# Kernel tuning notes

Measured on AMD Instinct MI355X. Metric: run time of the kernel, lower is better.

The kernel has to match this reference:

```python
import jax, jax.numpy as jnp
import numpy as np

N, E, G = 65536, 524288, 1024
ND, ED, HID, H, C = 21, 12, 128, 4, 32
L = 8  # num_blocks * 2 conv layers
EPS = 1e-5


def _gatv2(x, src, dst, ea, Wl, Wr, We, att, bias):
    # PyG GATv2Conv: xl=lin_l(x) (source), xr=lin_r(x) (target)
    n = x.shape[0]
    xl = jnp.einsum('nd,dhc->nhc', x, Wl)   # [N,H,C]
    xr = jnp.einsum('nd,dhc->nhc', x, Wr)
    el = jnp.einsum('ed,dhc->ehc', ea, We)  # [E,H,C]
    m = xl[src] + xr[dst] + el              # per-edge message pre-activation
    e = jnp.einsum('ehc,hc->eh', jax.nn.leaky_relu(m, 0.2), att)  # [E,H]
    # scatter softmax over incoming edges of each dst node
    emax = jax.ops.segment_max(e, dst, num_segments=n)
    emax = jnp.where(jnp.isfinite(emax), emax, 0.0)
    p = jnp.exp(e - emax[dst])
    denom = jax.ops.segment_sum(p, dst, num_segments=n)
    alpha = p / jnp.clip(denom, 1e-16)[dst]
    out = jax.ops.segment_sum(alpha[..., None] * xl[src], dst, num_segments=n)
    return out.reshape(n, H * C) + bias


def _bn(x, scale, bias):
    mu = x.mean(0)
    var = x.var(0)
    return (x - mu) * jax.lax.rsqrt(var + EPS) * scale + bias


def setup_inputs():
    key = jax.random.key(0)
    ks = jax.random.split(key, 16)
    f = lambda k, shp, s=0.05: jax.random.normal(k, shp, jnp.float32) * s
    return dict(
        x=f(ks[0], (N, ND), 1.0),
        edge_attr=f(ks[1], (E, ED), 1.0),
        edge_index=jax.random.randint(ks[2], (2, E), 0, N),
        batch=jnp.sort(jax.random.randint(ks[3], (N,), 0, G)),
        Win=f(ks[4], (ND, HID)), bin_=jnp.zeros(HID),
        Wl=f(ks[5], (L, HID, H, C)), Wr=f(ks[6], (L, HID, H, C)),
        We=f(ks[7], (L, ED, H, C)), att=f(ks[8], (L, H, C)),
        bconv=jnp.zeros((L, HID)),
        bn_scale=jnp.ones((L, HID)), bn_bias=jnp.zeros((L, HID)),
        Wv1=f(ks[9], (HID, 64)), bv1=jnp.zeros(64),
        Wv2=f(ks[10], (64, 3)), bv2=jnp.zeros(3),
        Wp1=f(ks[11], (2 * HID + ED, 64)), bp1=jnp.zeros(64),
        Wp2=f(ks[12], (64, 1)), bp2=jnp.zeros(1),
    )


def reference(x, edge_attr, edge_index, batch, Win, bin_, Wl, Wr, We, att,
              bconv, bn_scale, bn_bias, Wv1, bv1, Wv2, bv2, Wp1, bp1, Wp2, bp2):
    src0, dst0 = edge_index[0], edge_index[1]
    # add_self_loops with fill_value='mean' for edge features
    ones_e = jnp.ones((E,), x.dtype)
    deg = jax.ops.segment_sum(ones_e, dst0, num_segments=N)
    mean_ea = jax.ops.segment_sum(edge_attr, dst0, num_segments=N) / jnp.clip(deg, 1.0)[:, None]
    ar = jnp.arange(N)
    src = jnp.concatenate([src0, ar])
    dst = jnp.concatenate([dst0, ar])
    ea = jnp.concatenate([edge_attr, mean_ea], axis=0)

    h = jax.nn.relu(x @ Win + bin_)
    for b in range(L // 2):
        i, j = 2 * b, 2 * b + 1
        res = h
        h = _gatv2(h, src, dst, ea, Wl[i], Wr[i], We[i], att[i], bconv[i])
        h = jax.nn.relu(_bn(h, bn_scale[i], bn_bias[i]))
        h = _gatv2(h, src, dst, ea, Wl[j], Wr[j], We[j], att[j], bconv[j])
        h = _bn(h, bn_scale[j], bn_bias[j])
        h = jax.nn.relu(h + res)

    counts = jax.ops.segment_sum(jnp.ones((N,), h.dtype), batch, num_segments=G)
    pooled = jax.ops.segment_sum(h, batch, num_segments=G) / jnp.clip(counts, 1.0)[:, None]
    value_logits = jax.nn.relu(pooled @ Wv1 + bv1) @ Wv2 + bv2  # [G,3]

    edge_input = jnp.concatenate([h[src0], h[dst0], edge_attr], axis=1)  # [E, 2*HID+ED]
    policy_logits = (jax.nn.relu(edge_input @ Wp1 + bp1) @ Wp2 + bp2)[:, 0]  # [E]
    return value_logits, policy_logits
```

## Files before the change

### kernel.cpp

```cpp
#include <hip/hip_runtime.h>
#include <hip/hip_fp16.h>

#define NN 65536
#define EE 524288
#define EPX 589824
#define GG 1024
#define NSLOT 32

typedef __attribute__((ext_vector_type(8))) short bf16x8;
typedef __attribute__((ext_vector_type(4))) float f32x4;

#define LOG2E 1.44269504088896f


__device__ __forceinline__ unsigned short f2bf(float x) {
    unsigned int u = __float_as_uint(x);
    u += 0x7FFFu + ((u >> 16) & 1u);
    return (unsigned short)(u >> 16);
}
__device__ __forceinline__ float bflo(unsigned int w) { return __uint_as_float(w << 16); }
__device__ __forceinline__ float bfhi(unsigned int w) { return __uint_as_float(w & 0xFFFF0000u); }
__device__ __forceinline__ float bf2f(unsigned short u) { return __uint_as_float((unsigned int)u << 16); }
__device__ __forceinline__ float lrelu(float x) { return fmaf(0.4f, fabsf(x), 0.6f * x); }
__device__ __forceinline__ unsigned int packh2(float a, float b) {
    __half2 h = __floats2half2_rn(a, b);
    return *reinterpret_cast<unsigned int*>(&h);
}
__device__ __forceinline__ unsigned long long rfl64(unsigned long long v) {
    unsigned int lo = __builtin_amdgcn_readfirstlane((unsigned int)v);
    unsigned int hi = __builtin_amdgcn_readfirstlane((unsigned int)(v >> 32));
    return (((unsigned long long)hi) << 32) | lo;
}

template <int CTRL>
__device__ __forceinline__ float dpp_add(float v) {
    int x = __builtin_amdgcn_update_dpp(0, __float_as_int(v), CTRL, 0xf, 0xf, true);
    return v + __int_as_float(x);
}
__device__ __forceinline__ float head_reduce(float t) {
    t = dpp_add<0xB1>(t);
    t = dpp_add<0x4E>(t);
    t = dpp_add<0x124>(t);
    t = dpp_add<0x128>(t);
    return t;
}


__launch_bounds__(256)
__global__ void k_deg(const int* __restrict__ dst0, int* __restrict__ deg)
{
    int e = blockIdx.x * 256 + threadIdx.x;
    if (e >= EE) return;
    atomicAdd(&deg[dst0[e]], 1);
}

__launch_bounds__(1024)
__global__ void k_scan(const int* __restrict__ deg, int* __restrict__ rowptr)
{
    __shared__ int sums[1024];
    int t = threadIdx.x;
    int base = t * 64;
    int s = 0;
    for (int i = 0; i < 64; i++) s += deg[base + i] + 1;
    sums[t] = s;
    __syncthreads();
    for (int off = 1; off < 1024; off <<= 1) {
        int v = (t >= off) ? sums[t - off] : 0;
        __syncthreads();
        sums[t] += v;
        __syncthreads();
    }
    int off = sums[t] - s;
    for (int i = 0; i < 64; i++) { rowptr[base + i] = off; off += deg[base + i] + 1; }
    if (t == 1023) rowptr[NN] = off;
}

__launch_bounds__(256)
__global__ void k_scatter(const int* __restrict__ src0, const int* __restrict__ dst0,
                          const float* __restrict__ eattr,
                          const int* __restrict__ rowptr, const int* __restrict__ deg,
                          int* __restrict__ fill, int* __restrict__ csr_src,
                          unsigned short* __restrict__ eaCSR,
                          unsigned short* __restrict__ eaOrd)
{
    int e = blockIdx.x * 256 + threadIdx.x;
    if (e >= EPX) return;
    if (e < EE) {
        int d = dst0[e];
        int pos = rowptr[d] + atomicAdd(&fill[d], 1);
        csr_src[pos] = src0[e] << 8;
        const float* ep = eattr + (size_t)e * 12;
        float4 a = *reinterpret_cast<const float4*>(ep);
        float4 b = *reinterpret_cast<const float4*>(ep + 4);
        float4 c = *reinterpret_cast<const float4*>(ep + 8);
        uint4 w; w.x = packh2(a.x, a.y); w.y = packh2(a.z, a.w);
        w.z = packh2(b.x, b.y); w.w = packh2(b.z, b.w);
        uint2 w2 = make_uint2(packh2(c.x, c.y), packh2(c.z, c.w));
        unsigned short* o = eaCSR + (size_t)pos * 16;
        *reinterpret_cast<uint4*>(o) = w;
        *reinterpret_cast<uint2*>(o + 8) = w2;
        unsigned short* o2 = eaOrd + (size_t)e * 16;
        *reinterpret_cast<uint4*>(o2) = w;
        *reinterpret_cast<uint2*>(o2 + 8) = w2;
    } else {
        int n = e - EE;
        csr_src[rowptr[n] + deg[n]] = n << 8;
    }
}

__launch_bounds__(256)
__global__ void k_selfattr(const int* __restrict__ rowptr, unsigned short* __restrict__ eaCSR)
{
    int tid = blockIdx.x * 256 + threadIdx.x;
    int n = tid >> 4;
    int lk = tid & 15;
    if (lk >= 12) return;
    int beg = rowptr[n], endm1 = rowptr[n + 1] - 1;
    float s = 0.f;
    for (int p = beg; p < endm1; ++p) {
        __half h = *reinterpret_cast<const __half*>(&eaCSR[(size_t)p * 16 + lk]);
        s += __half2float(h);
    }
    float dv = fmaxf((float)(endm1 - beg), 1.0f);
    __half ho = __float2half(s / dv);
    eaCSR[(size_t)endm1 * 16 + lk] = *reinterpret_cast<unsigned short*>(&ho);
}


__launch_bounds__(256)
__global__ void k_wprep(const float* __restrict__ Wl, const float* __restrict__ Wr,
                        const float* __restrict__ Wp1,
                        unsigned short* __restrict__ wg, unsigned short* __restrict__ wp)
{
    int tid = blockIdx.x * 256 + threadIdx.x;
    if (tid < 32768) {
        int l = tid >> 12;
        int r = tid & 4095;
        int kt = r >> 10, ct = (r >> 6) & 15, lane = r & 63;
        int kb = kt * 32 + (lane >> 4) * 8;
        int col = ct * 16 + (lane & 15);
        const float* W = (col < 128) ? (Wl + (size_t)l * 16384 + col)
                                     : (Wr + (size_t)l * 16384 + (col - 128));
        unsigned short* o = wg + (size_t)tid * 8;
#pragma unroll
        for (int j = 0; j < 8; j++) o[j] = f2bf(W[(size_t)(kb + j) * 128]);
    } else if (tid < 34816) {
        int r = tid - 32768;
        int kt = r >> 9, ct = (r >> 6) & 7, lane = r & 63;
        int kb = kt * 32 + (lane >> 4) * 8;
        int col = ct * 16 + (lane & 15);
        const float* W = (col < 64) ? (Wp1 + col) : (Wp1 + 128 * 64 + (col - 64));
        unsigned short* o = wp + (size_t)r * 8;
#pragma unroll
        for (int j = 0; j < 8; j++) o[j] = f2bf(W[(size_t)(kb + j) * 64]);
    }
}


__launch_bounds__(256)
__global__ void k_input(const float* __restrict__ x, const float* __restrict__ Win,
                        const float* __restrict__ bin, float* __restrict__ h)
{
    __shared__ float W[21 * 128];
    int t = threadIdx.x;
    for (int i = t; i < 21 * 128; i += 256) W[i] = Win[i];
    __syncthreads();
    int c = t & 127, sub = t >> 7;
    int n0 = blockIdx.x * 16;
    float bc = bin[c];
    for (int i = 0; i < 8; i++) {
        int n = n0 + sub + i * 2;
        const float* xp = x + (size_t)n * 21;
        float acc = bc;
#pragma unroll
        for (int k = 0; k < 21; k++) acc = fmaf(xp[k], W[k * 128 + c], acc);
        h[(size_t)n * 128 + c] = fmaxf(acc, 0.f);
    }
}


__device__ __forceinline__ void load_afrag(const float* __restrict__ A, int arow, int kb,
                                           bf16x8 af[4])
{
#pragma unroll
    for (int kt = 0; kt < 4; kt++) {
        const float* ap = A + (size_t)arow * 128 + kt * 32 + kb;
        float4 lo = *reinterpret_cast<const float4*>(ap);
        float4 hi = *reinterpret_cast<const float4*>(ap + 4);
        bf16x8 v;
        v[0] = (short)f2bf(lo.x); v[1] = (short)f2bf(lo.y);
        v[2] = (short)f2bf(lo.z); v[3] = (short)f2bf(lo.w);
        v[4] = (short)f2bf(hi.x); v[5] = (short)f2bf(hi.y);
        v[6] = (short)f2bf(hi.z); v[7] = (short)f2bf(hi.w);
        af[kt] = v;
    }
}

__device__ __forceinline__ void gemm_gat_core(const bf16x8 af[4], const unsigned short* __restrict__ Bf,
                                              int row0, unsigned short* __restrict__ Cl,
                                              unsigned short* __restrict__ Cr, int lane)
{
    int crow = row0 + (lane >> 4) * 4;
    int c0 = lane & 15;
#pragma unroll
    for (int ct = 0; ct < 16; ct++) {
        f32x4 acc = {0.f, 0.f, 0.f, 0.f};
#pragma unroll
        for (int kt = 0; kt < 4; kt++) {
            bf16x8 bf = *reinterpret_cast<const bf16x8*>(Bf + ((size_t)(kt * 16 + ct) * 64 + lane) * 8);
            acc = __builtin_amdgcn_mfma_f32_16x16x32_bf16(af[kt], bf, acc, 0, 0, 0);
        }
        int col = ct * 16 + c0;
        unsigned short* C = (col < 128) ? Cl : Cr;
        int cc = col & 127;
#pragma unroll
        for (int r = 0; r < 4; r++)
            C[(size_t)(crow + r) * 128 + cc] = f2bf(acc[r]);
    }
}

__launch_bounds__(256)
__global__ void k_gemm_gat(const float* __restrict__ A, const unsigned short* __restrict__ Bf,
                           unsigned short* __restrict__ Cl, unsigned short* __restrict__ Cr)
{
    int wave = threadIdx.x >> 6, lane = threadIdx.x & 63;
    int row0 = blockIdx.x * 64 + wave * 16;
    bf16x8 af[4];
    load_afrag(A, row0 + (lane & 15), (lane >> 4) * 8, af);
    gemm_gat_core(af, Bf, row0, Cl, Cr, lane);
}

__launch_bounds__(256)
__global__ void k_gemm_gat_bn(const float* __restrict__ G, const float* __restrict__ bnstat,
                              const float* __restrict__ scale, const float* __restrict__ bias,
                              const unsigned short* __restrict__ Bf,
                              unsigned short* __restrict__ Cl, unsigned short* __restrict__ Cr)
{
    __shared__ float sA[128], bA[128];
    int t = threadIdx.x;
    if (t < 128) {
        float sum = 0.f, sq = 0.f;
#pragma unroll
        for (int sl = 0; sl < NSLOT; sl++) {
            sum += bnstat[sl * 256 + t];
            sq  += bnstat[sl * 256 + 128 + t];
        }
        const float invN = 1.0f / (float)NN;
        float mean = sum * invN;
        float var  = sq * invN - mean * mean;
        float sc   = scale[t] * rsqrtf(var + 1e-5f);
        sA[t] = sc;
        bA[t] = bias[t] - mean * sc;
    }
    __syncthreads();
    int wave = t >> 6, lane = t & 63;
    int row0 = blockIdx.x * 64 + wave * 16;
    int arow = row0 + (lane & 15);
    int kb = (lane >> 4) * 8;
    bf16x8 af[4];
#pragma unroll
    for (int kt = 0; kt < 4; kt++) {
        int cb = kt * 32 + kb;
        const float* gp = G + (size_t)arow * 128 + cb;
        float4 lo = *reinterpret_cast<const float4*>(gp);
        float4 hi = *reinterpret_cast<const float4*>(gp + 4);
        bf16x8 v;
        v[0] = (short)f2bf(fmaxf(fmaf(lo.x, sA[cb + 0], bA[cb + 0]), 0.f));
        v[1] = (short)f2bf(fmaxf(fmaf(lo.y, sA[cb + 1], bA[cb + 1]), 0.f));
        v[2] = (short)f2bf(fmaxf(fmaf(lo.z, sA[cb + 2], bA[cb + 2]), 0.f));
        v[3] = (short)f2bf(fmaxf(fmaf(lo.w, sA[cb + 3], bA[cb + 3]), 0.f));
        v[4] = (short)f2bf(fmaxf(fmaf(hi.x, sA[cb + 4], bA[cb + 4]), 0.f));
        v[5] = (short)f2bf(fmaxf(fmaf(hi.y, sA[cb + 5], bA[cb + 5]), 0.f));
        v[6] = (short)f2bf(fmaxf(fmaf(hi.z, sA[cb + 6], bA[cb + 6]), 0.f));
        v[7] = (short)f2bf(fmaxf(fmaf(hi.w, sA[cb + 7], bA[cb + 7]), 0.f));
        af[kt] = v;
    }
    gemm_gat_core(af, Bf, row0, Cl, Cr, lane);
}

__launch_bounds__(256)
__global__ void k_gemm_pol(const float* __restrict__ A, const unsigned short* __restrict__ Bf,
                           unsigned short* __restrict__ P)
{
    int wave = threadIdx.x >> 6, lane = threadIdx.x & 63;
    int row0 = blockIdx.x * 64 + wave * 16;
    bf16x8 af[4];
    load_afrag(A, row0 + (lane & 15), (lane >> 4) * 8, af);
    int crow = row0 + (lane >> 4) * 4;
    int c0 = lane & 15;
#pragma unroll
    for (int ct = 0; ct < 8; ct++) {
        f32x4 acc = {0.f, 0.f, 0.f, 0.f};
#pragma unroll
        for (int kt = 0; kt < 4; kt++) {
            bf16x8 bf = *reinterpret_cast<const bf16x8*>(Bf + ((size_t)(kt * 8 + ct) * 64 + lane) * 8);
            acc = __builtin_amdgcn_mfma_f32_16x16x32_bf16(af[kt], bf, acc, 0, 0, 0);
        }
        int col = ct * 16 + c0;
#pragma unroll
        for (int r = 0; r < 4; r++)
            P[(size_t)(crow + r) * 128 + col] = f2bf(acc[r]);
    }
}


__device__ __forceinline__ float2 edge_el(uint4 A, uint2 C,
                                          const __half2 wx[6], const __half2 wy[6])
{
    __half2 e0 = *reinterpret_cast<const __half2*>(&A.x);
    __half2 e1 = *reinterpret_cast<const __half2*>(&A.y);
    __half2 e2 = *reinterpret_cast<const __half2*>(&A.z);
    __half2 e3 = *reinterpret_cast<const __half2*>(&A.w);
    __half2 e4 = *reinterpret_cast<const __half2*>(&C.x);
    __half2 e5 = *reinterpret_cast<const __half2*>(&C.y);
    __half2 ax = __hmul2(e0, wx[0]);
    ax = __hfma2(e1, wx[1], ax); ax = __hfma2(e2, wx[2], ax);
    ax = __hfma2(e3, wx[3], ax); ax = __hfma2(e4, wx[4], ax);
    ax = __hfma2(e5, wx[5], ax);
    __half2 ay = __hmul2(e0, wy[0]);
    ay = __hfma2(e1, wy[1], ay); ay = __hfma2(e2, wy[2], ay);
    ay = __hfma2(e3, wy[3], ay); ay = __hfma2(e4, wy[4], ay);
    ay = __hfma2(e5, wy[5], ay);
    float2 r;
    r.x = __half2float(__hadd(__low2half(ax), __high2half(ax)));
    r.y = __half2float(__hadd(__low2half(ay), __high2half(ay)));
    return r;
}

__launch_bounds__(256)
__global__ void k_gat(const unsigned short* __restrict__ xlb, const unsigned short* __restrict__ xrb,
                      const unsigned short* __restrict__ eaCSR,
                      const int* __restrict__ rowptr, const int* __restrict__ csr_src,
                      const float* __restrict__ We, const float* __restrict__ att,
                      const float* __restrict__ bconv, float* __restrict__ g,
                      float* __restrict__ bnstat)
{
    int wid = blockIdx.x * 4 + (threadIdx.x >> 6);
    int lane = threadIdx.x & 63;
    int f0 = lane * 2;

    const int* cs_s = (const int*)rfl64((unsigned long long)csr_src);
    const unsigned short* ea_s = (const unsigned short*)rfl64((unsigned long long)eaCSR);

    __half2 wx[6], wy[6];
#pragma unroll
    for (int j = 0; j < 6; j++) {
        float2 w0 = *reinterpret_cast<const float2*>(We + (2 * j) * 128 + f0);
        float2 w1 = *reinterpret_cast<const float2*>(We + (2 * j + 1) * 128 + f0);
        wx[j] = __floats2half2_rn(w0.x, w1.x);
        wy[j] = __floats2half2_rn(w0.y, w1.y);
    }
    float2 av = *reinterpret_cast<const float2*>(att + f0);
    av.x *= LOG2E; av.y *= LOG2E;
    float2 bc = *reinterpret_cast<const float2*>(bconv + f0);
    const char* xl_lane = reinterpret_cast<const char*>(xlb) + (lane << 2);

    float bs0 = 0.f, bs1 = 0.f, bq0 = 0.f, bq1 = 0.f;

    for (int n = wid * 4; n < wid * 4 + 4; ++n) {
        unsigned int xrw = *reinterpret_cast<const unsigned int*>(xrb + (size_t)n * 128 + f0);
        float xr0 = bflo(xrw), xr1 = bfhi(xrw);

        float sA_ = 0.f, a0A = 0.f, a1A = 0.f;
        float sB_ = 0.f, a0B = 0.f, a1B = 0.f;
        int beg = rowptr[n], end = rowptr[n + 1];
        int idx = beg;
        for (; idx + 4 <= end; idx += 4) {
            int off0 = cs_s[idx],     off1 = cs_s[idx + 1];
            int off2 = cs_s[idx + 2], off3 = cs_s[idx + 3];
            const unsigned short* ep = ea_s + (size_t)idx * 16;
            uint4 qA = *reinterpret_cast<const uint4*>(ep);
            uint2 qC = *reinterpret_cast<const uint2*>(ep + 8);
            uint4 rA = *reinterpret_cast<const uint4*>(ep + 16);
            uint2 rC = *reinterpret_cast<const uint2*>(ep + 24);
            uint4 sAq = *reinterpret_cast<const uint4*>(ep + 32);
            uint2 sC = *reinterpret_cast<const uint2*>(ep + 40);
            uint4 tA = *reinterpret_cast<const uint4*>(ep + 48);
            uint2 tC = *reinterpret_cast<const uint2*>(ep + 56);
            unsigned int xw0 = *reinterpret_cast<const unsigned int*>(xl_lane + off0);
            unsigned int xw1 = *reinterpret_cast<const unsigned int*>(xl_lane + off1);
            unsigned int xw2 = *reinterpret_cast<const unsigned int*>(xl_lane + off2);
            unsigned int xw3 = *reinterpret_cast<const unsigned int*>(xl_lane + off3);

            float2 el0 = edge_el(qA, qC, wx, wy);
            float2 el1 = edge_el(rA, rC, wx, wy);
            float2 el2 = edge_el(sAq, sC, wx, wy);
            float2 el3 = edge_el(tA, tC, wx, wy);

            float xa0 = bflo(xw0), xa1 = bfhi(xw0);
            float xb0 = bflo(xw1), xb1 = bfhi(xw1);
            float xc0 = bflo(xw2), xc1 = bfhi(xw2);
            float xd0 = bflo(xw3), xd1 = bfhi(xw3);

            float t0 = lrelu(xa0 + xr0 + el0.x) * av.x + lrelu(xa1 + xr1 + el0.y) * av.y;
            float t1 = lrelu(xb0 + xr0 + el1.x) * av.x + lrelu(xb1 + xr1 + el1.y) * av.y;
            float t2 = lrelu(xc0 + xr0 + el2.x) * av.x + lrelu(xc1 + xr1 + el2.y) * av.y;
            float t3 = lrelu(xd0 + xr0 + el3.x) * av.x + lrelu(xd1 + xr1 + el3.y) * av.y;
            t0 = head_reduce(t0); t1 = head_reduce(t1);
            t2 = head_reduce(t2); t3 = head_reduce(t3);

            float w0 = exp2f(t0);
            float w1 = exp2f(t1);
            float w2 = exp2f(t2);
            float w3 = exp2f(t3);
            sA_ += w0 + w1;
            sB_ += w2 + w3;
            a0A = fmaf(w0, xa0, fmaf(w1, xb0, a0A));
            a1A = fmaf(w0, xa1, fmaf(w1, xb1, a1A));
            a0B = fmaf(w2, xc0, fmaf(w3, xd0, a0B));
            a1B = fmaf(w2, xc1, fmaf(w3, xd1, a1B));
        }
        for (; idx < end; ++idx) {
            int off0 = cs_s[idx];
            const unsigned short* ep = ea_s + (size_t)idx * 16;
            uint4 qA = *reinterpret_cast<const uint4*>(ep);
            uint2 qC = *reinterpret_cast<const uint2*>(ep + 8);
            unsigned int xw0 = *reinterpret_cast<const unsigned int*>(xl_lane + off0);
            float2 el0 = edge_el(qA, qC, wx, wy);
            float xa0 = bflo(xw0), xa1 = bfhi(xw0);
            float tt = lrelu(xa0 + xr0 + el0.x) * av.x + lrelu(xa1 + xr1 + el0.y) * av.y;
            tt = head_reduce(tt);
            float w = exp2f(tt);
            sA_ += w;
            a0A = fmaf(w, xa0, a0A);
            a1A = fmaf(w, xa1, a1A);
        }
        float s  = sA_ + sB_;
        float a0 = a0A + a0B;
        float a1 = a1A + a1B;
        float inv = 1.f / s;
        float r0 = fmaf(a0, inv, bc.x);
        float r1 = fmaf(a1, inv, bc.y);
        *reinterpret_cast<float2*>(g + (size_t)n * 128 + f0) = make_float2(r0, r1);
        bs0 += r0; bs1 += r1;
        bq0 = fmaf(r0, r0, bq0); bq1 = fmaf(r1, r1, bq1);
    }

    __shared__ float red[256 * 4];
    int t = threadIdx.x;
    red[t * 4 + 0] = bs0; red[t * 4 + 1] = bs1;
    red[t * 4 + 2] = bq0; red[t * 4 + 3] = bq1;
    __syncthreads();
    if (t < 64) {
        float v0 = red[t * 4 + 0] + red[(t + 64) * 4 + 0] + red[(t + 128) * 4 + 0] + red[(t + 192) * 4 + 0];
        float v1 = red[t * 4 + 1] + red[(t + 64) * 4 + 1] + red[(t + 128) * 4 + 1] + red[(t + 192) * 4 + 1];
        float q0 = red[t * 4 + 2] + red[(t + 64) * 4 + 2] + red[(t + 128) * 4 + 2] + red[(t + 192) * 4 + 2];
        float q1 = red[t * 4 + 3] + red[(t + 64) * 4 + 3] + red[(t + 128) * 4 + 3] + red[(t + 192) * 4 + 3];
        float* slot = bnstat + (size_t)(blockIdx.x & (NSLOT - 1)) * 256;
        atomicAdd(&slot[2 * t + 0], v0);
        atomicAdd(&slot[2 * t + 1], v1);
        atomicAdd(&slot[128 + 2 * t + 0], q0);
        atomicAdd(&slot[128 + 2 * t + 1], q1);
    }
}


__launch_bounds__(256)
__global__ void k_bnapply_res_relu(const float4* __restrict__ gin,
                                   const float* __restrict__ bnstat,
                                   const float* __restrict__ scale, const float* __restrict__ bias,
                                   float4* __restrict__ hbuf)
{
    __shared__ float sA[128], bA[128];
    int t = threadIdx.x;
    if (t < 128) {
        float sum = 0.f, sq = 0.f;
#pragma unroll
        for (int sl = 0; sl < NSLOT; sl++) {
            sum += bnstat[sl * 256 + t];
            sq  += bnstat[sl * 256 + 128 + t];
        }
        const float invN = 1.0f / (float)NN;
        float mean = sum * invN;
        float var  = sq * invN - mean * mean;
        float sc   = scale[t] * rsqrtf(var + 1e-5f);
        sA[t] = sc;
        bA[t] = bias[t] - mean * sc;
    }
    __syncthreads();
    int idx = blockIdx.x * 256 + t;
    int c4 = (idx & 31) * 4;
    float4 v = gin[idx];
    float4 hv = hbuf[idx];
    float4 r;
    r.x = fmaxf(fmaf(v.x, sA[c4 + 0], bA[c4 + 0]) + hv.x, 0.f);
    r.y = fmaxf(fmaf(v.y, sA[c4 + 1], bA[c4 + 1]) + hv.y, 0.f);
    r.z = fmaxf(fmaf(v.z, sA[c4 + 2], bA[c4 + 2]) + hv.z, 0.f);
    r.w = fmaxf(fmaf(v.w, sA[c4 + 3], bA[c4 + 3]) + hv.w, 0.f);
    hbuf[idx] = r;
}


__launch_bounds__(128)
__global__ void k_pool(const float* __restrict__ h, const int* __restrict__ batch,
                       float* __restrict__ pooled, float* __restrict__ cnt)
{
    int c = threadIdx.x;
    int r0 = blockIdx.x * 128;
    int cur = batch[r0];
    float acc = 0.f;
    float run = 0.f;
    for (int i = 0; i < 128; ++i) {
        int r = r0 + i;
        int b = batch[r];
        if (b != cur) {
            atomicAdd(&pooled[(size_t)cur * 128 + c], acc);
            if (c == 0) atomicAdd(&cnt[cur], run);
            acc = 0.f; run = 0.f; cur = b;
        }
        acc += h[(size_t)r * 128 + c];
        run += 1.f;
    }
    atomicAdd(&pooled[(size_t)cur * 128 + c], acc);
    if (c == 0) atomicAdd(&cnt[cur], run);
}

__launch_bounds__(64)
__global__ void k_value(const float* __restrict__ pooled, const float* __restrict__ cnt,
                        const float* __restrict__ Wv1, const float* __restrict__ bv1,
                        const float* __restrict__ Wv2, const float* __restrict__ bv2,
                        float* __restrict__ out)
{
    int gi = blockIdx.x;
    int l = threadIdx.x;
    float inv = 1.f / fmaxf(cnt[gi], 1.f);
    const float* pr = pooled + (size_t)gi * 128;
    float z = bv1[l];
    for (int k = 0; k < 128; k++) z = fmaf(pr[k] * inv, Wv1[k * 64 + l], z);
    z = fmaxf(z, 0.f);
#pragma unroll
    for (int j = 0; j < 3; j++) {
        float p = z * Wv2[l * 3 + j];
        p += __shfl_xor(p, 32); p += __shfl_xor(p, 16); p += __shfl_xor(p, 8);
        p += __shfl_xor(p, 4);  p += __shfl_xor(p, 2);  p += __shfl_xor(p, 1);
        if (l == 0) out[gi * 3 + j] = p + bv2[j];
    }
}


__device__ __forceinline__ void dec12(uint4 A, uint2 C, float* o)
{
    __half2 h;
    h = *reinterpret_cast<__half2*>(&A.x); o[0] = __low2float(h); o[1]  = __high2float(h);
    h = *reinterpret_cast<__half2*>(&A.y); o[2] = __low2float(h); o[3]  = __high2float(h);
    h = *reinterpret_cast<__half2*>(&A.z); o[4] = __low2float(h); o[5]  = __high2float(h);
    h = *reinterpret_cast<__half2*>(&A.w); o[6] = __low2float(h); o[7]  = __high2float(h);
    h = *reinterpret_cast<__half2*>(&C.x); o[8] = __low2float(h); o[9]  = __high2float(h);
    h = *reinterpret_cast<__half2*>(&C.y); o[10] = __low2float(h); o[11] = __high2float(h);
}

__launch_bounds__(256)
__global__ void k_policy(const unsigned short* __restrict__ P,
                         const unsigned short* __restrict__ eaOrd,
                         const int* __restrict__ src0, const int* __restrict__ dst0,
                         const float* __restrict__ Wp1c, const float* __restrict__ bp1,
                         const float* __restrict__ Wp2, const float* __restrict__ bp2,
                         float* __restrict__ out)
{
    int wave = (blockIdx.x * 256 + threadIdx.x) >> 6;
    int lane = threadIdx.x & 63;
    const unsigned short* ea_s = (const unsigned short*)rfl64((unsigned long long)eaOrd);
    const int* s_s = (const int*)rfl64((unsigned long long)src0);
    const int* d_s = (const int*)rfl64((unsigned long long)dst0);
    float w1c[12];
#pragma unroll
    for (int k = 0; k < 12; k++) w1c[k] = Wp1c[k * 64 + lane];
    float wp2 = Wp2[lane];
    float bb = bp1[lane];
    float b2 = bp2[0];
    for (int i = 0; i < 8; i += 2) {
        int e0i = wave * 8 + i;
        int e1i = e0i + 1;
        int sI0 = s_s[e0i], dI0 = d_s[e0i];
        int sI1 = s_s[e1i], dI1 = d_s[e1i];
        const unsigned short* ep = ea_s + (size_t)e0i * 16;
        uint4 A0 = *reinterpret_cast<const uint4*>(ep);
        uint2 C0 = *reinterpret_cast<const uint2*>(ep + 8);
        uint4 A1 = *reinterpret_cast<const uint4*>(ep + 16);
        uint2 C1 = *reinterpret_cast<const uint2*>(ep + 24);
        unsigned short ps0 = P[(size_t)sI0 * 128 + lane];
        unsigned short pd0 = P[(size_t)dI0 * 128 + 64 + lane];
        unsigned short ps1 = P[(size_t)sI1 * 128 + lane];
        unsigned short pd1 = P[(size_t)dI1 * 128 + 64 + lane];

        float ea0[12], ea1[12];
        dec12(A0, C0, ea0);
        dec12(A1, C1, ea1);

        float z0 = bf2f(ps0) + bf2f(pd0) + bb;
        float z1 = bf2f(ps1) + bf2f(pd1) + bb;
#pragma unroll
        for (int k = 0; k < 12; k++) {
            z0 = fmaf(ea0[k], w1c[k], z0);
            z1 = fmaf(ea1[k], w1c[k], z1);
        }
        float p0 = fmaxf(z0, 0.f) * wp2;
        float p1 = fmaxf(z1, 0.f) * wp2;
        p0 = head_reduce(p0);
        p1 = head_reduce(p1);
        p0 += __shfl_xor(p0, 16); p1 += __shfl_xor(p1, 16);
        p0 += __shfl_xor(p0, 32); p1 += __shfl_xor(p1, 32);
        if (lane == 0) {
            out[3072 + e0i] = p0 + b2;
            out[3072 + e1i] = p1 + b2;
        }
    }
}


extern "C" void kernel_launch(void* const* d_in, const int* in_sizes, int n_in,
                              void* d_out, int out_size, void* d_ws, size_t ws_size,
                              hipStream_t stream)
{
    const float* x     = (const float*)d_in[0];
    const float* eattr = (const float*)d_in[1];
    const int*   eidx  = (const int*)d_in[2];
    const int*   batch = (const int*)d_in[3];
    const float* Win   = (const float*)d_in[4];
    const float* bin   = (const float*)d_in[5];
    const float* Wl    = (const float*)d_in[6];
    const float* Wr    = (const float*)d_in[7];
    const float* We    = (const float*)d_in[8];
    const float* att   = (const float*)d_in[9];
    const float* bconv = (const float*)d_in[10];
    const float* bnsc  = (const float*)d_in[11];
    const float* bnbi  = (const float*)d_in[12];
    const float* Wv1   = (const float*)d_in[13];
    const float* bv1   = (const float*)d_in[14];
    const float* Wv2   = (const float*)d_in[15];
    const float* bv2   = (const float*)d_in[16];
    const float* Wp1   = (const float*)d_in[17];
    const float* bp1   = (const float*)d_in[18];
    const float* Wp2   = (const float*)d_in[19];
    const float* bp2   = (const float*)d_in[20];
    float* out = (float*)d_out;

    const int* src0 = eidx;
    const int* dst0 = eidx + EE;

    const size_t NH = (size_t)NN * 128;
    float* ws = (float*)d_ws;
    float* h  = ws;
    float* g  = h + NH;
    unsigned short* xlb = (unsigned short*)(g + NH);
    unsigned short* xrb = xlb + NH;
    unsigned short* eaCSR = xrb + NH;
    unsigned short* eaOrd = eaCSR + (size_t)EPX * 16;
    int* rowptr = (int*)(eaOrd + (size_t)EE * 16);
    int* csr_src = rowptr + (NN + 1);
    int* deg  = csr_src + EPX;
    int* fill = deg + NN;
    float* bnstat = (float*)(fill + NN);
    float* pooled = bnstat + 8 * NSLOT * 256;
    float* cnt    = pooled + (size_t)GG * 128;
    size_t zero_elems = (size_t)NN + NN + 8 * NSLOT * 256 + (size_t)GG * 128 + GG;
    unsigned short* wg = (unsigned short*)(cnt + GG);
    unsigned short* wp = wg + 8 * 32768;

    hipMemsetAsync(deg, 0, zero_elems * sizeof(float), stream);

    k_deg<<<EE / 256, 256, 0, stream>>>(dst0, deg);
    k_scan<<<1, 1024, 0, stream>>>(deg, rowptr);
    k_scatter<<<EPX / 256, 256, 0, stream>>>(src0, dst0, eattr, rowptr, deg, fill,
                                             csr_src, eaCSR, eaOrd);
    k_selfattr<<<(NN * 16) / 256, 256, 0, stream>>>(rowptr, eaCSR);
    k_wprep<<<136, 256, 0, stream>>>(Wl, Wr, Wp1, wg, wp);

    k_input<<<NN / 16, 256, 0, stream>>>(x, Win, bin, h);

    for (int l = 0; l < 8; l++) {
        float* bs = bnstat + (size_t)l * NSLOT * 256;
        if (l % 2 == 0) {
            k_gemm_gat<<<NN / 64, 256, 0, stream>>>(h, wg + (size_t)l * 32768, xlb, xrb);
        } else {
            float* bsp = bnstat + (size_t)(l - 1) * NSLOT * 256;
            k_gemm_gat_bn<<<NN / 64, 256, 0, stream>>>(g, bsp,
                                                       bnsc + (size_t)(l - 1) * 128,
                                                       bnbi + (size_t)(l - 1) * 128,
                                                       wg + (size_t)l * 32768, xlb, xrb);
        }
        k_gat<<<NN / 16, 256, 0, stream>>>(xlb, xrb, eaCSR, rowptr, csr_src,
                                           We + (size_t)l * 1536, att + (size_t)l * 128,
                                           bconv + (size_t)l * 128, g, bs);
        if (l % 2 == 1) {
            k_bnapply_res_relu<<<(NN * 128 / 4) / 256, 256, 0, stream>>>(
                (const float4*)g, bs, bnsc + (size_t)l * 128, bnbi + (size_t)l * 128,
                (float4*)h);
        }
    }

    k_pool<<<NN / 128, 128, 0, stream>>>(h, batch, pooled, cnt);
    k_value<<<GG, 64, 0, stream>>>(pooled, cnt, Wv1, bv1, Wv2, bv2, out);

    unsigned short* P = xlb;
    k_gemm_pol<<<NN / 64, 256, 0, stream>>>(h, wp, P);
    k_policy<<<NN / 4, 256, 0, stream>>>(P, eaOrd, src0, dst0,
                                         Wp1 + 256 * 64, bp1, Wp2, bp2, out);
}
```

Baseline: 1.082 ms.

## Fuse BN-residual-ReLU into next GEMM and use fdot2 for edge features

```diff
diff --git a/kernel.cpp b/kernel.cpp
--- a/kernel.cpp
+++ b/kernel.cpp
@@ -9,8 +9,13 @@
 
 typedef __attribute__((ext_vector_type(8))) short bf16x8;
 typedef __attribute__((ext_vector_type(4))) float f32x4;
+typedef _Float16 f16x2 __attribute__((ext_vector_type(2)));
 
 #define LOG2E 1.44269504088896f
+
+#if __has_builtin(__builtin_amdgcn_fdot2)
+#define HAVE_FDOT2 1
+#endif
 
 
 __device__ __forceinline__ unsigned short f2bf(float x) {
@@ -25,6 +30,17 @@
 __device__ __forceinline__ unsigned int packh2(float a, float b) {
     __half2 h = __floats2half2_rn(a, b);
     return *reinterpret_cast<unsigned int*>(&h);
+}
+__device__ __forceinline__ f16x2 as_f16x2(unsigned int u) {
+    union { unsigned int u; f16x2 h; } c; c.u = u; return c.h;
+}
+__device__ __forceinline__ float fdot2p(unsigned int e, f16x2 w, float acc) {
+#ifdef HAVE_FDOT2
+    return __builtin_amdgcn_fdot2(as_f16x2(e), w, acc, false);
+#else
+    __half2 h = *reinterpret_cast<__half2*>(&e);
+    return acc + __low2float(h) * (float)w[0] + __high2float(h) * (float)w[1];
+#endif
 }
 __device__ __forceinline__ unsigned long long rfl64(unsigned long long v) {
     unsigned int lo = __builtin_amdgcn_readfirstlane((unsigned int)v);
@@ -230,13 +246,11 @@
     gemm_gat_core(af, Bf, row0, Cl, Cr, lane);
 }
 
-__launch_bounds__(256)
-__global__ void k_gemm_gat_bn(const float* __restrict__ G, const float* __restrict__ bnstat,
-                              const float* __restrict__ scale, const float* __restrict__ bias,
-                              const unsigned short* __restrict__ Bf,
-                              unsigned short* __restrict__ Cl, unsigned short* __restrict__ Cr)
-{
-    __shared__ float sA[128], bA[128];
+__device__ __forceinline__ void bn_coeff_lds(const float* __restrict__ bnstat,
+                                             const float* __restrict__ scale,
+                                             const float* __restrict__ bias,
+                                             float* sA, float* bA)
+{
     int t = threadIdx.x;
     if (t < 128) {
         float sum = 0.f, sq = 0.f;
@@ -253,6 +267,17 @@
         bA[t] = bias[t] - mean * sc;
     }
     __syncthreads();
+}
+
+__launch_bounds__(256)
+__global__ void k_gemm_gat_bn(const float* __restrict__ G, const float* __restrict__ bnstat,
+                              const float* __restrict__ scale, const float* __restrict__ bias,
+                              const unsigned short* __restrict__ Bf,
+                              unsigned short* __restrict__ Cl, unsigned short* __restrict__ Cr)
+{
+    __shared__ float sA[128], bA[128];
+    bn_coeff_lds(bnstat, scale, bias, sA, bA);
+    int t = threadIdx.x;
     int wave = t >> 6, lane = t & 63;
     int row0 = blockIdx.x * 64 + wave * 16;
     int arow = row0 + (lane & 15);
@@ -279,6 +304,50 @@
 }
 
 __launch_bounds__(256)
+__global__ void k_gemm_gat_bnres(const float* __restrict__ G, const float* __restrict__ bnstat,
+                                 const float* __restrict__ scale, const float* __restrict__ bias,
+                                 float* __restrict__ H, const unsigned short* __restrict__ Bf,
+                                 unsigned short* __restrict__ Cl, unsigned short* __restrict__ Cr)
+{
+    __shared__ float sA[128], bA[128];
+    bn_coeff_lds(bnstat, scale, bias, sA, bA);
+    int t = threadIdx.x;
+    int wave = t >> 6, lane = t & 63;
+    int row0 = blockIdx.x * 64 + wave * 16;
+    int arow = row0 + (lane & 15);
+    int kb = (lane >> 4) * 8;
+    bf16x8 af[4];
+#pragma unroll
+    for (int kt = 0; kt < 4; kt++) {
+        int cb = kt * 32 + kb;
+        const float* gp = G + (size_t)arow * 128 + cb;
+        float* hp = H + (size_t)arow * 128 + cb;
+        float4 glo = *reinterpret_cast<const float4*>(gp);
+        float4 ghi = *reinterpret_cast<const float4*>(gp + 4);
+        float4 hlo = *reinterpret_cast<const float4*>(hp);
+        float4 hhi = *reinterpret_cast<const float4*>(hp + 4);
+        float4 nlo, nhi;
+        nlo.x = fmaxf(fmaf(glo.x, sA[cb + 0], bA[cb + 0]) + hlo.x, 0.f);
+        nlo.y = fmaxf(fmaf(glo.y, sA[cb + 1], bA[cb + 1]) + hlo.y, 0.f);
+        nlo.z = fmaxf(fmaf(glo.z, sA[cb + 2], bA[cb + 2]) + hlo.z, 0.f);
+        nlo.w = fmaxf(fmaf(glo.w, sA[cb + 3], bA[cb + 3]) + hlo.w, 0.f);
+        nhi.x = fmaxf(fmaf(ghi.x, sA[cb + 4], bA[cb + 4]) + hhi.x, 0.f);
+        nhi.y = fmaxf(fmaf(ghi.y, sA[cb + 5], bA[cb + 5]) + hhi.y, 0.f);
+        nhi.z = fmaxf(fmaf(ghi.z, sA[cb + 6], bA[cb + 6]) + hhi.z, 0.f);
+        nhi.w = fmaxf(fmaf(ghi.w, sA[cb + 7], bA[cb + 7]) + hhi.w, 0.f);
+        *reinterpret_cast<float4*>(hp) = nlo;
+        *reinterpret_cast<float4*>(hp + 4) = nhi;
+        bf16x8 v;
+        v[0] = (short)f2bf(nlo.x); v[1] = (short)f2bf(nlo.y);
+        v[2] = (short)f2bf(nlo.z); v[3] = (short)f2bf(nlo.w);
+        v[4] = (short)f2bf(nhi.x); v[5] = (short)f2bf(nhi.y);
+        v[6] = (short)f2bf(nhi.z); v[7] = (short)f2bf(nhi.w);
+        af[kt] = v;
+    }
+    gemm_gat_core(af, Bf, row0, Cl, Cr, lane);
+}
+
+__launch_bounds__(256)
 __global__ void k_gemm_pol(const float* __restrict__ A, const unsigned short* __restrict__ Bf,
                            unsigned short* __restrict__ P)
 {
@@ -305,25 +374,21 @@
 
 
 __device__ __forceinline__ float2 edge_el(uint4 A, uint2 C,
-                                          const __half2 wx[6], const __half2 wy[6])
-{
-    __half2 e0 = *reinterpret_cast<const __half2*>(&A.x);
-    __half2 e1 = *reinterpret_cast<const __half2*>(&A.y);
-    __half2 e2 = *reinterpret_cast<const __half2*>(&A.z);
-    __half2 e3 = *reinterpret_cast<const __half2*>(&A.w);
-    __half2 e4 = *reinterpret_cast<const __half2*>(&C.x);
-    __half2 e5 = *reinterpret_cast<const __half2*>(&C.y);
-    __half2 ax = __hmul2(e0, wx[0]);
-    ax = __hfma2(e1, wx[1], ax); ax = __hfma2(e2, wx[2], ax);
-    ax = __hfma2(e3, wx[3], ax); ax = __hfma2(e4, wx[4], ax);
-    ax = __hfma2(e5, wx[5], ax);
-    __half2 ay = __hmul2(e0, wy[0]);
-    ay = __hfma2(e1, wy[1], ay); ay = __hfma2(e2, wy[2], ay);
-    ay = __hfma2(e3, wy[3], ay); ay = __hfma2(e4, wy[4], ay);
-    ay = __hfma2(e5, wy[5], ay);
-    float2 r;
-    r.x = __half2float(__hadd(__low2half(ax), __high2half(ax)));
-    r.y = __half2float(__hadd(__low2half(ay), __high2half(ay)));
+                                          const f16x2 wx[6], const f16x2 wy[6])
+{
+    float ex = fdot2p(A.x, wx[0], 0.f);
+    ex = fdot2p(A.y, wx[1], ex);
+    ex = fdot2p(A.z, wx[2], ex);
+    ex = fdot2p(A.w, wx[3], ex);
+    ex = fdot2p(C.x, wx[4], ex);
+    ex = fdot2p(C.y, wx[5], ex);
+    float ey = fdot2p(A.x, wy[0], 0.f);
+    ey = fdot2p(A.y, wy[1], ey);
+    ey = fdot2p(A.z, wy[2], ey);
+    ey = fdot2p(A.w, wy[3], ey);
+    ey = fdot2p(C.x, wy[4], ey);
+    ey = fdot2p(C.y, wy[5], ey);
+    float2 r; r.x = ex; r.y = ey;
     return r;
 }
 
@@ -342,13 +407,13 @@
     const int* cs_s = (const int*)rfl64((unsigned long long)csr_src);
     const unsigned short* ea_s = (const unsigned short*)rfl64((unsigned long long)eaCSR);
 
-    __half2 wx[6], wy[6];
+    f16x2 wx[6], wy[6];
 #pragma unroll
     for (int j = 0; j < 6; j++) {
         float2 w0 = *reinterpret_cast<const float2*>(We + (2 * j) * 128 + f0);
         float2 w1 = *reinterpret_cast<const float2*>(We + (2 * j + 1) * 128 + f0);
-        wx[j] = __floats2half2_rn(w0.x, w1.x);
-        wy[j] = __floats2half2_rn(w0.y, w1.y);
+        wx[j] = (f16x2){(_Float16)w0.x, (_Float16)w1.x};
+        wy[j] = (f16x2){(_Float16)w0.y, (_Float16)w1.y};
     }
     float2 av = *reinterpret_cast<const float2*>(att + f0);
     av.x *= LOG2E; av.y *= LOG2E;
@@ -462,22 +527,8 @@
                                    float4* __restrict__ hbuf)
 {
     __shared__ float sA[128], bA[128];
+    bn_coeff_lds(bnstat, scale, bias, sA, bA);
     int t = threadIdx.x;
-    if (t < 128) {
-        float sum = 0.f, sq = 0.f;
-#pragma unroll
-        for (int sl = 0; sl < NSLOT; sl++) {
-            sum += bnstat[sl * 256 + t];
-            sq  += bnstat[sl * 256 + 128 + t];
-        }
-        const float invN = 1.0f / (float)NN;
-        float mean = sum * invN;
-        float var  = sq * invN - mean * mean;
-        float sc   = scale[t] * rsqrtf(var + 1e-5f);
-        sA[t] = sc;
-        bA[t] = bias[t] - mean * sc;
-    }
-    __syncthreads();
     int idx = blockIdx.x * 256 + t;
     int c4 = (idx & 31) * 4;
     float4 v = gin[idx];
@@ -538,17 +589,6 @@
 }
 
 
-__device__ __forceinline__ void dec12(uint4 A, uint2 C, float* o)
-{
-    __half2 h;
-    h = *reinterpret_cast<__half2*>(&A.x); o[0] = __low2float(h); o[1]  = __high2float(h);
-    h = *reinterpret_cast<__half2*>(&A.y); o[2] = __low2float(h); o[3]  = __high2float(h);
-    h = *reinterpret_cast<__half2*>(&A.z); o[4] = __low2float(h); o[5]  = __high2float(h);
-    h = *reinterpret_cast<__half2*>(&A.w); o[6] = __low2float(h); o[7]  = __high2float(h);
-    h = *reinterpret_cast<__half2*>(&C.x); o[8] = __low2float(h); o[9]  = __high2float(h);
-    h = *reinterpret_cast<__half2*>(&C.y); o[10] = __low2float(h); o[11] = __high2float(h);
-}
-
 __launch_bounds__(256)
 __global__ void k_policy(const unsigned short* __restrict__ P,
                          const unsigned short* __restrict__ eaOrd,
@@ -562,9 +602,10 @@
     const unsigned short* ea_s = (const unsigned short*)rfl64((unsigned long long)eaOrd);
     const int* s_s = (const int*)rfl64((unsigned long long)src0);
     const int* d_s = (const int*)rfl64((unsigned long long)dst0);
-    float w1c[12];
-#pragma unroll
-    for (int k = 0; k < 12; k++) w1c[k] = Wp1c[k * 64 + lane];
+    f16x2 w1h[6];
+#pragma unroll
+    for (int j = 0; j < 6; j++)
+        w1h[j] = (f16x2){(_Float16)Wp1c[(2 * j) * 64 + lane], (_Float16)Wp1c[(2 * j + 1) * 64 + lane]};
     float wp2 = Wp2[lane];
     float bb = bp1[lane];
     float b2 = bp2[0];
@@ -583,17 +624,15 @@
         unsigned short ps1 = P[(size_t)sI1 * 128 + lane];
         unsigned short pd1 = P[(size_t)dI1 * 128 + 64 + lane];
 
-        float ea0[12], ea1[12];
-        dec12(A0, C0, ea0);
-        dec12(A1, C1, ea1);
-
         float z0 = bf2f(ps0) + bf2f(pd0) + bb;
+        z0 = fdot2p(A0.x, w1h[0], z0); z0 = fdot2p(A0.y, w1h[1], z0);
+        z0 = fdot2p(A0.z, w1h[2], z0); z0 = fdot2p(A0.w, w1h[3], z0);
+        z0 = fdot2p(C0.x, w1h[4], z0); z0 = fdot2p(C0.y, w1h[5], z0);
         float z1 = bf2f(ps1) + bf2f(pd1) + bb;
-#pragma unroll
-        for (int k = 0; k < 12; k++) {
-            z0 = fmaf(ea0[k], w1c[k], z0);
-            z1 = fmaf(ea1[k], w1c[k], z1);
-        }
+        z1 = fdot2p(A1.x, w1h[0], z1); z1 = fdot2p(A1.y, w1h[1], z1);
+        z1 = fdot2p(A1.z, w1h[2], z1); z1 = fdot2p(A1.w, w1h[3], z1);
+        z1 = fdot2p(C1.x, w1h[4], z1); z1 = fdot2p(C1.y, w1h[5], z1);
+
         float p0 = fmaxf(z0, 0.f) * wp2;
         float p1 = fmaxf(z1, 0.f) * wp2;
         p0 = head_reduce(p0);
@@ -670,19 +709,25 @@
 
     for (int l = 0; l < 8; l++) {
         float* bs = bnstat + (size_t)l * NSLOT * 256;
-        if (l % 2 == 0) {
-            k_gemm_gat<<<NN / 64, 256, 0, stream>>>(h, wg + (size_t)l * 32768, xlb, xrb);
-        } else {
+        if (l == 0) {
+            k_gemm_gat<<<NN / 64, 256, 0, stream>>>(h, wg, xlb, xrb);
+        } else if (l % 2 == 1) {
             float* bsp = bnstat + (size_t)(l - 1) * NSLOT * 256;
             k_gemm_gat_bn<<<NN / 64, 256, 0, stream>>>(g, bsp,
                                                        bnsc + (size_t)(l - 1) * 128,
                                                        bnbi + (size_t)(l - 1) * 128,
                                                        wg + (size_t)l * 32768, xlb, xrb);
+        } else {
+            float* bsp = bnstat + (size_t)(l - 1) * NSLOT * 256;
+            k_gemm_gat_bnres<<<NN / 64, 256, 0, stream>>>(g, bsp,
+                                                          bnsc + (size_t)(l - 1) * 128,
+                                                          bnbi + (size_t)(l - 1) * 128,
+                                                          h, wg + (size_t)l * 32768, xlb, xrb);
         }
         k_gat<<<NN / 16, 256, 0, stream>>>(xlb, xrb, eaCSR, rowptr, csr_src,
                                            We + (size_t)l * 1536, att + (size_t)l * 128,
                                            bconv + (size_t)l * 128, g, bs);
-        if (l % 2 == 1) {
+        if (l == 7) {
             k_bnapply_res_relu<<<(NN * 128 / 4) / 256, 256, 0, stream>>>(
                 (const float4*)g, bs, bnsc + (size_t)l * 128, bnbi + (size_t)l * 128,
                 (float4*)h);
```

New measurement: 1.043 ms, median of 2. 3.6% less time.
